# Kernel tuning notes

Measured on AMD Instinct MI355X. Metric: run time of the kernel, lower is better.

The kernel has to match this reference:

```python
import jax, jax.numpy as jnp
import numpy as np

EPS_L2 = 1e-6
EPS_RMS = 1e-6

def _dw_causal(x, w):
    # depthwise causal conv: x [B,L,C], w [C,K] (torch Conv1d weight [C,1,K] squeezed)
    K = w.shape[1]
    L = x.shape[1]
    xp = jnp.pad(x, ((0, 0), (K - 1, 0), (0, 0)))
    out = jnp.zeros_like(x)
    for j in range(K):  # K=4, fixed small kernel
        out = out + w[:, j] * xp[:, j:j + L, :]
    return out

def _qkv_conv(x, dw, pw):
    # depthwise causal conv -> pointwise 1x1 conv -> SiLU
    return jax.nn.silu(_dw_causal(x, dw) @ pw.T)

def _l2n(x):
    return x / (jnp.linalg.norm(x, axis=-1, keepdims=True) + EPS_L2)

def setup_inputs() -> dict:
    key = jax.random.key(0)
    B, L, D, M, P, K = 2, 1024, 2048, 2048, 8, 4
    ks = jax.random.split(key, 16)
    inp = {}
    inp['x'] = jax.random.normal(ks[0], (B, L, D), dtype=jnp.float32)
    inp['Wq'] = jax.random.normal(ks[1], (M, D), dtype=jnp.float32) * 0.02
    inp['Wk'] = jax.random.normal(ks[2], (M, D), dtype=jnp.float32) * 0.02
    inp['Wv'] = jax.random.normal(ks[3], (M, D), dtype=jnp.float32) * 0.02
    inp['q_dw'] = jax.random.normal(ks[4], (M, K), dtype=jnp.float32) * 0.1
    inp['k_dw'] = jax.random.normal(ks[5], (M, K), dtype=jnp.float32) * 0.1
    inp['v_dw'] = jax.random.normal(ks[6], (M, K), dtype=jnp.float32) * 0.1
    inp['q_pw'] = jax.random.normal(ks[7], (M, M), dtype=jnp.float32) * 0.02
    inp['k_pw'] = jax.random.normal(ks[8], (M, M), dtype=jnp.float32) * 0.02
    inp['v_pw'] = jax.random.normal(ks[9], (M, M), dtype=jnp.float32) * 0.02
    inp['pk'] = jax.random.normal(ks[10], (P, M), dtype=jnp.float32) * 0.02
    inp['pv'] = jax.random.normal(ks[11], (P, M), dtype=jnp.float32) * 0.02
    inp['mlp_w1'] = jnp.eye(M, dtype=jnp.float32) * 0.1
    inp['mlp_w2'] = jnp.eye(M, dtype=jnp.float32) * 0.1
    inp['eta_w'] = jnp.zeros((1, D), dtype=jnp.float32)
    inp['eta_b'] = jnp.full((1,), 2.0, dtype=jnp.float32)
    inp['theta_w'] = jnp.zeros((1, D), dtype=jnp.float32)
    inp['theta_b'] = jnp.full((1,), -1.0, dtype=jnp.float32)
    inp['alpha_w'] = jnp.zeros((1, D), dtype=jnp.float32)
    inp['alpha_b'] = jnp.full((1,), -2.0, dtype=jnp.float32)
    inp['gate_w'] = jax.random.normal(ks[12], (M, M), dtype=jnp.float32) * 0.02
    inp['gate_b'] = jnp.zeros((M,), dtype=jnp.float32)
    inp['out_w'] = jax.random.normal(ks[13], (D, M), dtype=jnp.float32) * 0.02
    inp['ln_w'] = jnp.ones((D,), dtype=jnp.float32)
    inp['mem_state'] = jnp.zeros((M, M), dtype=jnp.float32)
    inp['sur_state'] = jnp.zeros((M, M), dtype=jnp.float32)
    return inp

def reference(x, Wq, Wk, Wv, q_dw, q_pw, k_dw, k_pw, v_dw, v_pw, pk, pv,
              mlp_w1, mlp_w2, eta_w, eta_b, theta_w, theta_b, alpha_w, alpha_b,
              gate_w, gate_b, out_w, ln_w, mem_state, sur_state):
    B, L, D = x.shape
    M = Wq.shape[0]
    P = pk.shape[0]
    # projections + causal depthwise-separable convs + SiLU
    q = _qkv_conv(x @ Wq.T, q_dw, q_pw)
    k = _qkv_conv(x @ Wk.T, k_dw, k_pw)
    v = _qkv_conv(x @ Wv.T, v_dw, v_pw)
    q = _l2n(q)
    k = _l2n(k)
    # data-dependent eta/theta/alpha from mean-pooled input, scalarized
    x_pooled = x.mean(axis=1)  # [B, D]
    eta = jax.nn.sigmoid(x_pooled @ eta_w.T + eta_b).mean()
    theta = jax.nn.sigmoid(x_pooled @ theta_w.T + theta_b).mean()
    alpha = jax.nn.sigmoid(x_pooled @ alpha_w.T + alpha_b).mean()
    # persistent memory tokens
    pk_n = _l2n(pk)
    k_wp = jnp.concatenate([jnp.broadcast_to(pk_n[None], (B, P, M)), k], axis=1)
    v_wp = jnp.concatenate([jnp.broadcast_to(pv[None], (B, P, M)), v], axis=1)
    # test-time memory update (torch.no_grad block -> stop_gradient)
    pred = jnp.einsum('blm,mh->blh', k, mem_state)
    err = v - pred
    momentary = jnp.einsum('bld,blh->dh', k, err) / (B * L)
    new_surprise = eta * sur_state + theta * momentary
    new_memory = (1.0 - alpha) * mem_state + new_surprise
    snapshot = jax.lax.stop_gradient(new_memory)
    # retrieval: linear memory + deep memory MLP
    linear_ret = jnp.einsum('blm,mh->blh', q, snapshot)
    mlp_ret = jax.nn.silu(q @ mlp_w1.T) @ mlp_w2.T
    retrieved = linear_ret + mlp_ret
    # causal attention with always-visible persistent tokens
    scores = jnp.einsum('blm,bpm->blp', q, k_wp) / jnp.sqrt(jnp.float32(M))
    col = jnp.arange(P + L)
    row = jnp.arange(L)
    mask = (col[None, :] < P) | ((col[None, :] - P) <= row[:, None])  # [L, P+L]
    scores = jnp.where(mask[None], scores, -jnp.inf)
    attn = jax.nn.softmax(scores.astype(jnp.float32), axis=-1).astype(x.dtype)
    context = jnp.einsum('blp,bpm->blm', attn, v_wp)
    retrieved = retrieved + context
    # gated output projection + residual + RMSNorm
    gate = jax.nn.sigmoid(retrieved @ gate_w.T + gate_b)
    out = x + (gate * retrieved) @ out_w.T
    rms = jnp.sqrt(jnp.mean(out * out, axis=-1, keepdims=True) + EPS_RMS)
    return (out / rms) * ln_w
```

## Files before the change

### kernel.cpp

```cpp
#include <hip/hip_runtime.h>
#include <hip/hip_bf16.h>


#define NROWS 2048
#define MD    2048
#define PL    1032
#define PLP   1152
#define NM    4194304

using bf16x8 = __attribute__((ext_vector_type(8))) __bf16;
using f32x4  = __attribute__((ext_vector_type(4))) float;
using u16x8  = __attribute__((ext_vector_type(8))) unsigned short;

__device__ __forceinline__ unsigned short f2bf(float f) {
    union { float f; unsigned int u; } c; c.f = f;
    unsigned int u = c.u;
    return (unsigned short)((u + 0x7fffu + ((u >> 16) & 1u)) >> 16);
}
__device__ __forceinline__ float bf2f(unsigned short h) {
    union { float f; unsigned int u; } c; c.u = ((unsigned int)h) << 16;
    return c.f;
}
__device__ __forceinline__ float ldf(const float* p) { return *p; }
__device__ __forceinline__ float ldf(const unsigned short* p) { return bf2f(*p); }
__device__ __forceinline__ float sigm(float x) { return 1.f / (1.f + __expf(-x)); }
__device__ __forceinline__ float silu(float x) { return x / (1.f + __expf(-x)); }

__device__ __forceinline__ float block_reduce_sum(float v) {
    __shared__ float ws[4];
    #pragma unroll
    for (int o = 32; o > 0; o >>= 1) v += __shfl_down(v, o);
    __syncthreads();
    if ((threadIdx.x & 63) == 0) ws[threadIdx.x >> 6] = v;
    __syncthreads();
    return (ws[0] + ws[1]) + (ws[2] + ws[3]);
}
__device__ __forceinline__ float block_reduce_max(float v) {
    __shared__ float wm[4];
    #pragma unroll
    for (int o = 32; o > 0; o >>= 1) v = fmaxf(v, __shfl_down(v, o));
    __syncthreads();
    if ((threadIdx.x & 63) == 0) wm[threadIdx.x >> 6] = v;
    __syncthreads();
    return fmaxf(fmaxf(wm[0], wm[1]), fmaxf(wm[2], wm[3]));
}

__device__ __forceinline__ void load_lds16(const unsigned short* g, unsigned short* l) {
    __builtin_amdgcn_global_load_lds(
        (const __attribute__((address_space(1))) unsigned int*)g,
        (__attribute__((address_space(3))) unsigned int*)l, 16, 0, 0);
}
__device__ __forceinline__ void raw_barrier() {
    __asm__ volatile("" ::: "memory");
    __builtin_amdgcn_s_barrier();
    __asm__ volatile("" ::: "memory");
}
__device__ __forceinline__ void epi_store(int epi, float* Cf, unsigned short* Ch,
                                          long off, float v) {
    if (epi == 0)      Cf[off] = v;
    else if (epi == 1) Cf[off] += v;
    else if (epi == 2) Ch[off] = f2bf(v);
    else               Ch[off] = f2bf(silu(v));
}

__global__ __launch_bounds__(256) void gemm_nt(
    const unsigned short* __restrict__ A, const unsigned short* __restrict__ Bm,
    void* __restrict__ Cv, int Mc, int K, long sA, long sB, long sCb, int epiPack)
{
    __shared__ unsigned short As[2][8192];
    __shared__ unsigned short Bs[2][4096];
    const int tid = threadIdx.x, lane = tid & 63, w = tid >> 6;
    const int l16 = lane & 15, quad = lane >> 4;
    const int wr = (w >> 1) * 64, wc = (w & 1) * 32;
    const long rowBase = (long)blockIdx.y * 128;
    const long colBase = (long)blockIdx.x * 64;
    const unsigned short* Ap = A + (long)blockIdx.z * sA;
    const unsigned short* Bp = Bm + (long)blockIdx.z * sB;
    const int epi = (epiPack >> (blockIdx.z * 4)) & 15;
    const int r8 = lane >> 3;
    const int cg = (lane & 7) ^ r8;

    const unsigned short* gA[4]; const unsigned short* gB[2];
    unsigned short* lA[4]; unsigned short* lB[2];
    #pragma unroll
    for (int t = 0; t < 4; ++t) {
        int ch = w * 4 + t;
        gA[t] = Ap + (rowBase + ch * 8 + r8) * (long)K + cg * 8;
        lA[t] = &As[0][ch * 512];
    }
    #pragma unroll
    for (int t = 0; t < 2; ++t) {
        int ch = w * 2 + t;
        gB[t] = Bp + (colBase + ch * 8 + r8) * (long)K + cg * 8;
        lB[t] = &Bs[0][ch * 512];
    }

    f32x4 acc[4][2] = {};
    #pragma unroll
    for (int t = 0; t < 4; ++t) { load_lds16(gA[t], lA[t]); gA[t] += 64; }
    #pragma unroll
    for (int t = 0; t < 2; ++t) { load_lds16(gB[t], lB[t]); gB[t] += 64; }

    const int nIter = K >> 6;
    for (int it = 0; it < nIter; ++it) {
        const int cb = it & 1;
        if (it + 1 < nIter) {
            const int nb = cb ^ 1;
            #pragma unroll
            for (int t = 0; t < 4; ++t) { load_lds16(gA[t], lA[t] + nb * 8192); gA[t] += 64; }
            #pragma unroll
            for (int t = 0; t < 2; ++t) { load_lds16(gB[t], lB[t] + nb * 4096); gB[t] += 64; }
            __builtin_amdgcn_s_waitcnt(0xF76);
        } else {
            __builtin_amdgcn_s_waitcnt(0xF70);
        }
        raw_barrier();
        const unsigned short* Ac = As[cb];
        const unsigned short* Bc = Bs[cb];
        #pragma unroll
        for (int ks = 0; ks < 2; ++ks) {
            const int cl = ((ks * 4 + quad) ^ (l16 & 7)) * 8;
            bf16x8 af[4], bfr[2];
            #pragma unroll
            for (int i = 0; i < 4; ++i)
                af[i] = *(const bf16x8*)&Ac[(wr + i * 16 + l16) * 64 + cl];
            #pragma unroll
            for (int j = 0; j < 2; ++j)
                bfr[j] = *(const bf16x8*)&Bc[(wc + j * 16 + l16) * 64 + cl];
            #pragma unroll
            for (int i = 0; i < 4; ++i)
                #pragma unroll
                for (int j = 0; j < 2; ++j)
                    acc[i][j] = __builtin_amdgcn_mfma_f32_16x16x32_bf16(af[i], bfr[j], acc[i][j], 0, 0, 0);
        }
        raw_barrier();
    }

    char* Cb = (char*)Cv + (long)blockIdx.z * sCb;
    float* Cf = (float*)Cb;
    unsigned short* Ch = (unsigned short*)Cb;
    #pragma unroll
    for (int i = 0; i < 4; ++i)
        #pragma unroll
        for (int r = 0; r < 4; ++r) {
            long gr = rowBase + wr + i * 16 + quad * 4 + r;
            #pragma unroll
            for (int j = 0; j < 2; ++j) {
                long gc = colBase + wc + j * 16 + l16;
                epi_store(epi, Cf, Ch, gr * (long)Mc + gc, acc[i][j][r]);
            }
        }
}

#define G256_RD_A(p)                                                            \
    _Pragma("unroll") for (int fr = 0; fr < 2; ++fr)                            \
    _Pragma("unroll") for (int ks = 0; ks < 2; ++ks)                            \
        af[fr][ks] = *(const bf16x8*)&Ac[(wr + ((p) * 2 + fr) * 16 + l16) * 64  \
                                         + ((ks * 4 + quad) ^ (l16 & 7)) * 8];
#define G256_MFMA(p)                                                            \
    __builtin_amdgcn_s_setprio(1);                                              \
    _Pragma("unroll") for (int ks = 0; ks < 2; ++ks)                            \
    _Pragma("unroll") for (int fr = 0; fr < 2; ++fr)                            \
    _Pragma("unroll") for (int fc = 0; fc < 4; ++fc)                            \
        acc[(p) * 2 + fr][fc] = __builtin_amdgcn_mfma_f32_16x16x32_bf16(        \
            af[fr][ks], bfr[fc][ks], acc[(p) * 2 + fr][fc], 0, 0, 0);           \
    __builtin_amdgcn_s_setprio(0);
#define G256_STG_A(h)                                                           \
    do { load_lds16(gA[h][0], &Anx[lofs[h][0]]); gA[h][0] += 64;                \
         load_lds16(gA[h][1], &Anx[lofs[h][1]]); gA[h][1] += 64; } while (0)
#define G256_STG_B(h)                                                           \
    do { load_lds16(gB[h][0], &Bnx[lofs[h][0]]); gB[h][0] += 64;                \
         load_lds16(gB[h][1], &Bnx[lofs[h][1]]); gB[h][1] += 64; } while (0)

__global__ __launch_bounds__(512, 2) void gemm_nt_256(
    const unsigned short* __restrict__ A, const unsigned short* __restrict__ Bm,
    void* __restrict__ Cv, int Mc, int K, long sA, long sB, long sCb, int epiPack)
{
    __shared__ unsigned short As[2][16384];
    __shared__ unsigned short Bs[2][16384];
    const int tid = threadIdx.x, lane = tid & 63, w = tid >> 6;
    const int l16 = lane & 15, quad = lane >> 4;
    const int wr = (w >> 2) * 128, wc = (w & 3) * 64;
    const long rowBase = (long)blockIdx.y * 256;
    const long colBase = (long)blockIdx.x * 256;
    const unsigned short* Ap = A + (long)blockIdx.z * sA;
    const unsigned short* Bp = Bm + (long)blockIdx.z * sB;
    const int epi = (epiPack >> (blockIdx.z * 4)) & 15;
    const int r8 = lane >> 3;
    const int cg = (lane & 7) ^ r8;

    const unsigned short* gA[2][2]; const unsigned short* gB[2][2];
    int lofs[2][2];
    #pragma unroll
    for (int h = 0; h < 2; ++h)
        #pragma unroll
        for (int j = 0; j < 2; ++j) {
            const int rowOff = h * 128 + j * 64 + w * 8 + r8;
            gA[h][j] = Ap + (rowBase + rowOff) * (long)K + cg * 8;
            gB[h][j] = Bp + (colBase + rowOff) * (long)K + cg * 8;
            lofs[h][j] = (h * 128 + j * 64 + w * 8) * 64;
        }

    const int nT = K >> 6;
    f32x4 acc[8][4] = {};

    #pragma unroll
    for (int h = 0; h < 2; ++h)
        #pragma unroll
        for (int j = 0; j < 2; ++j) { load_lds16(gA[h][j], &As[0][lofs[h][j]]); gA[h][j] += 64; }
    #pragma unroll
    for (int h = 0; h < 2; ++h)
        #pragma unroll
        for (int j = 0; j < 2; ++j) { load_lds16(gB[h][j], &Bs[0][lofs[h][j]]); gB[h][j] += 64; }
    if (nT > 1) {
        #pragma unroll
        for (int h = 0; h < 2; ++h)
            #pragma unroll
            for (int j = 0; j < 2; ++j) { load_lds16(gB[h][j], &Bs[1][lofs[h][j]]); gB[h][j] += 64; }
        __builtin_amdgcn_s_waitcnt(0x0F74);
    } else {
        __builtin_amdgcn_s_waitcnt(0x0F70);
    }
    raw_barrier();

    for (int t = 0; t < nT; ++t) {
        const int cb = t & 1;
        const unsigned short* Ac = As[cb];
        const unsigned short* Bc = Bs[cb];
        unsigned short* Anx = As[cb ^ 1];
        unsigned short* Bnx = Bs[cb];
        const bool stA = (t + 1 < nT);
        const bool stB = (t + 2 < nT);
        bf16x8 bfr[4][2];
        bf16x8 af[2][2];

        #pragma unroll
        for (int fc = 0; fc < 4; ++fc)
            #pragma unroll
            for (int ks = 0; ks < 2; ++ks)
                bfr[fc][ks] = *(const bf16x8*)&Bc[(wc + fc * 16 + l16) * 64
                                                 + ((ks * 4 + quad) ^ (l16 & 7)) * 8];
        G256_RD_A(0)
        if (stA) G256_STG_A(0);
        raw_barrier();
        G256_MFMA(0)
        raw_barrier();

        G256_RD_A(1)
        if (stA) G256_STG_A(1);
        raw_barrier();
        G256_MFMA(1)
        raw_barrier();

        G256_RD_A(2)
        if (stB) G256_STG_B(0);
        raw_barrier();
        G256_MFMA(2)
        raw_barrier();

        G256_RD_A(3)
        if (stB) {
            G256_STG_B(1);
            __builtin_amdgcn_s_waitcnt(0x0F74);
        } else {
            __builtin_amdgcn_s_waitcnt(0x0F70);
        }
        raw_barrier();
        G256_MFMA(3)
        raw_barrier();
    }

    char* Cb = (char*)Cv + (long)blockIdx.z * sCb;
    float* Cf = (float*)Cb;
    unsigned short* Ch = (unsigned short*)Cb;
    #pragma unroll
    for (int i = 0; i < 8; ++i)
        #pragma unroll
        for (int r = 0; r < 4; ++r) {
            long gr = rowBase + wr + i * 16 + quad * 4 + r;
            #pragma unroll
            for (int j = 0; j < 4; ++j) {
                long gc = colBase + wc + j * 16 + l16;
                epi_store(epi, Cf, Ch, gr * (long)Mc + gc, acc[i][j][r]);
            }
        }
}

template <typename TS>
__global__ void k_transpose(const TS* __restrict__ src, unsigned short* __restrict__ dst,
                            int R, int C, int dstLd, int dstOff, long sSrc, long sDst)
{
    __shared__ float tile[32][33];
    const TS* sp = src + (long)blockIdx.z * sSrc;
    unsigned short* dp = dst + (long)blockIdx.z * sDst;
    int c0 = blockIdx.x * 32, r0 = blockIdx.y * 32;
    int tx = threadIdx.x, ty = threadIdx.y;
    #pragma unroll
    for (int i = 0; i < 4; ++i)
        tile[ty + i * 8][tx] = ldf(&sp[(long)(r0 + ty + i * 8) * C + c0 + tx]);
    __syncthreads();
    #pragma unroll
    for (int i = 0; i < 4; ++i)
        dp[(long)(c0 + ty + i * 8) * dstLd + dstOff + r0 + tx] = f2bf(tile[tx][ty + i * 8]);
}

__global__ void k_errT_kT(const unsigned short* __restrict__ vf, const float* __restrict__ pred,
                          const unsigned short* __restrict__ k_bf, unsigned short* __restrict__ eT)
{
    __shared__ float tile[32][33];
    int z = blockIdx.z;
    int c0 = blockIdx.x * 32, r0 = blockIdx.y * 32;
    int tx = threadIdx.x, ty = threadIdx.y;
    #pragma unroll
    for (int i = 0; i < 4; ++i) {
        long idx = (long)(r0 + ty + i * 8) * MD + c0 + tx;
        tile[ty + i * 8][tx] = (z == 0) ? (bf2f(vf[idx]) - pred[idx]) : bf2f(k_bf[idx]);
    }
    __syncthreads();
    unsigned short* dst = eT + (long)z * NM;
    #pragma unroll
    for (int i = 0; i < 4; ++i)
        dst[(long)(c0 + ty + i * 8) * MD + r0 + tx] = f2bf(tile[tx][ty + i * 8]);
}

__global__ void k_snapT(const float* __restrict__ mem, const float* __restrict__ sur,
                        const float* __restrict__ momT, const float* __restrict__ scal,
                        unsigned short* __restrict__ dst)
{
    __shared__ float tile[32][33];
    float eta = scal[0], theta = scal[1], alpha = scal[2];
    int h0 = blockIdx.y * 32, d0 = blockIdx.x * 32;
    int tx = threadIdx.x, ty = threadIdx.y;
    #pragma unroll
    for (int i = 0; i < 4; ++i) {
        long idx = (long)(d0 + ty + i * 8) * MD + h0 + tx;
        tile[ty + i * 8][tx] = (1.f - alpha) * mem[idx] + eta * sur[idx];
    }
    __syncthreads();
    #pragma unroll
    for (int i = 0; i < 4; ++i) {
        long oidx = (long)(h0 + ty + i * 8) * MD + d0 + tx;
        dst[oidx] = f2bf(tile[tx][ty + i * 8] + theta * (1.f / 2048.f) * momT[oidx]);
    }
}

__global__ void k_cvt_multi(const float* s0, const float* s1, const float* s2, const float* s3,
                            const float* s4, const float* s5, const float* s6, const float* s7,
                            unsigned short* d0, unsigned short* d1, unsigned short* d2, unsigned short* d3,
                            unsigned short* d4, unsigned short* d5, unsigned short* d6, unsigned short* d7)
{
    int seg = blockIdx.x >> 11;
    const float* s; unsigned short* d;
    switch (seg) {
        case 0: s = s0; d = d0; break;  case 1: s = s1; d = d1; break;
        case 2: s = s2; d = d2; break;  case 3: s = s3; d = d3; break;
        case 4: s = s4; d = d4; break;  case 5: s = s5; d = d5; break;
        case 6: s = s6; d = d6; break;  default: s = s7; d = d7; break;
    }
    long idx = ((long)(blockIdx.x & 2047) * 256 + threadIdx.x) * 8;
    float4 a = *(const float4*)(s + idx);
    float4 b = *(const float4*)(s + idx + 4);
    u16x8 o;
    o[0] = f2bf(a.x); o[1] = f2bf(a.y); o[2] = f2bf(a.z); o[3] = f2bf(a.w);
    o[4] = f2bf(b.x); o[5] = f2bf(b.y); o[6] = f2bf(b.z); o[7] = f2bf(b.w);
    *(u16x8*)(d + idx) = o;
}

__global__ void k_dwconv(const unsigned short* __restrict__ tproj,
                         const float* __restrict__ qdw, const float* __restrict__ kdw,
                         const float* __restrict__ vdw, unsigned short* __restrict__ conv)
{
    long u = (long)blockIdx.x * 256 + threadIdx.x;
    long flat = u * 8;
    int z = (int)(flat >> 22);
    int rem = (int)(flat & (NM - 1));
    int n = rem >> 11, m = rem & 2047;
    int l = n & 1023;
    const float* dw = (z == 0) ? qdw : (z == 1) ? kdw : vdw;
    const unsigned short* src = tproj + (long)n * 6144 + z * 2048 + m;
    float4 dwv[8];
    #pragma unroll
    for (int e = 0; e < 8; ++e) dwv[e] = *(const float4*)(dw + (m + e) * 4);
    float acc[8] = {};
    #pragma unroll
    for (int j = 0; j < 4; ++j) {
        int dl = j - 3;
        if (l + dl >= 0) {
            u16x8 r = *(const u16x8*)(src + (long)dl * 6144);
            #pragma unroll
            for (int e = 0; e < 8; ++e)
                acc[e] += ((const float*)&dwv[e])[j] * bf2f(r[e]);
        }
    }
    u16x8 o;
    #pragma unroll
    for (int e = 0; e < 8; ++e) o[e] = f2bf(acc[e]);
    *(u16x8*)(conv + (long)z * NM + (long)n * 2048 + m) = o;
}

__global__ void k_post_qkv(const float* __restrict__ t_big, unsigned short* __restrict__ q_bf,
                           unsigned short* __restrict__ k_bf, unsigned short* __restrict__ vf,
                           unsigned short* __restrict__ kwp)
{
    int bid = blockIdx.x, z = bid >> 11, n = bid & 2047;
    const float* row = t_big + (long)z * NM + (long)n * 2048;
    int t = threadIdx.x;
    float4 a = *(const float4*)(row + t * 8);
    float4 b = *(const float4*)(row + t * 8 + 4);
    float v[8] = {silu(a.x), silu(a.y), silu(a.z), silu(a.w),
                  silu(b.x), silu(b.y), silu(b.z), silu(b.w)};
    if (z == 2) {
        u16x8 o;
        #pragma unroll
        for (int e = 0; e < 8; ++e) o[e] = f2bf(v[e]);
        *(u16x8*)(vf + (long)n * 2048 + t * 8) = o;
        return;
    }
    float ss = 0.f;
    #pragma unroll
    for (int e = 0; e < 8; ++e) ss += v[e] * v[e];
    ss = block_reduce_sum(ss);
    float inv = 1.f / (sqrtf(ss) + 1e-6f);
    u16x8 o;
    #pragma unroll
    for (int e = 0; e < 8; ++e) o[e] = f2bf(v[e] * inv);
    if (z == 0) {
        *(u16x8*)(q_bf + (long)n * 2048 + t * 8) = o;
    } else {
        *(u16x8*)(k_bf + (long)n * 2048 + t * 8) = o;
        int bb = n >> 10, l = n & 1023;
        *(u16x8*)(kwp + ((long)bb * PLP + 8 + l) * MD + t * 8) = o;
    }
}

__global__ void k_misc(const float* __restrict__ pk, const float* __restrict__ pv,
                       unsigned short* __restrict__ kwp, unsigned short* __restrict__ vwpT)
{
    int bid = blockIdx.x, t = threadIdx.x;
    if (bid < 8) {
        const float* row = pk + bid * MD;
        float4 a = *(const float4*)(row + t * 8);
        float4 b = *(const float4*)(row + t * 8 + 4);
        float v[8] = {a.x, a.y, a.z, a.w, b.x, b.y, b.z, b.w};
        float ss = 0.f;
        #pragma unroll
        for (int e = 0; e < 8; ++e) ss += v[e] * v[e];
        ss = block_reduce_sum(ss);
        float inv = 1.f / (sqrtf(ss) + 1e-6f);
        u16x8 o;
        #pragma unroll
        for (int e = 0; e < 8; ++e) o[e] = f2bf(v[e] * inv);
        *(u16x8*)(kwp + (long)bid * MD + t * 8) = o;
        *(u16x8*)(kwp + (long)PLP * MD + (long)bid * MD + t * 8) = o;
    } else if (bid < 72) {
        int i = (bid - 8) * 256 + t;
        int m = i >> 3, pp = i & 7;
        unsigned short h = f2bf(pv[pp * MD + m]);
        vwpT[(long)m * PLP + pp] = h;
        vwpT[(long)MD * PLP + (long)m * PLP + pp] = h;
    } else if (bid < 312) {
        long flat = ((long)(bid - 72) * 256 + t) * 8;
        int b = (int)(flat / 245760);
        int r = (int)(flat % 245760);
        int j = 1032 + (r >> 11), m = r & 2047;
        u16x8 zz = {};
        *(u16x8*)(kwp + ((long)b * PLP + j) * MD + m) = zz;
    } else {
        long flat = ((long)(bid - 312) * 256 + t) * 8;
        int bm = (int)(flat / 120);
        int o = (int)(flat % 120);
        u16x8 zz = {};
        *(u16x8*)(vwpT + (long)bm * PLP + 1032 + o) = zz;
    }
}

__global__ void k_pooled(const float* __restrict__ x, const float* __restrict__ ew,
                         const float* __restrict__ tw, const float* __restrict__ aw,
                         float* __restrict__ dots) {
    int b = blockIdx.y;
    long base = (long)b * 1024 * MD;
    long start = (long)blockIdx.x * 8192;
    float s0 = 0, s1 = 0, s2 = 0;
    for (int s = 0; s < 32; ++s) {
        long f = start + threadIdx.x + (long)s * 256;
        float xv = x[base + f];
        int d = (int)(f & (MD - 1));
        s0 += xv * ew[d]; s1 += xv * tw[d]; s2 += xv * aw[d];
    }
    s0 = block_reduce_sum(s0);
    if (threadIdx.x == 0) atomicAdd(&dots[0 + b], s0);
    s1 = block_reduce_sum(s1);
    if (threadIdx.x == 0) atomicAdd(&dots[2 + b], s1);
    s2 = block_reduce_sum(s2);
    if (threadIdx.x == 0) atomicAdd(&dots[4 + b], s2);
}
__global__ void k_scal_fin(const float* __restrict__ dots, const float* __restrict__ eb,
                           const float* __restrict__ tb, const float* __restrict__ ab,
                           float* __restrict__ scal) {
    if (threadIdx.x == 0 && blockIdx.x == 0) {
        const float invL = 1.f / 1024.f;
        float e = 0, th = 0, al = 0;
        for (int b = 0; b < 2; ++b) {
            e  += sigm(dots[0 + b] * invL + eb[0]);
            th += sigm(dots[2 + b] * invL + tb[0]);
            al += sigm(dots[4 + b] * invL + ab[0]);
        }
        scal[0] = e * 0.5f; scal[1] = th * 0.5f; scal[2] = al * 0.5f;
    }
}

__global__ void k_addcvt(const float* __restrict__ a, const float* __restrict__ b,
                         unsigned short* __restrict__ o) {
    long i = ((long)blockIdx.x * 256 + threadIdx.x) * 8;
    float4 a0 = *(const float4*)(a + i), a1 = *(const float4*)(a + i + 4);
    float4 b0 = *(const float4*)(b + i), b1 = *(const float4*)(b + i + 4);
    u16x8 r;
    r[0] = f2bf(a0.x + b0.x); r[1] = f2bf(a0.y + b0.y); r[2] = f2bf(a0.z + b0.z); r[3] = f2bf(a0.w + b0.w);
    r[4] = f2bf(a1.x + b1.x); r[5] = f2bf(a1.y + b1.y); r[6] = f2bf(a1.z + b1.z); r[7] = f2bf(a1.w + b1.w);
    *(u16x8*)(o + i) = r;
}
__global__ void k_gate8(const float* __restrict__ pre, const float* __restrict__ gb,
                        const float* __restrict__ ret, const float* __restrict__ mlp2,
                        unsigned short* __restrict__ o) {
    long i = ((long)blockIdx.x * 256 + threadIdx.x) * 8;
    int m = (int)(i & (MD - 1));
    float4 p0 = *(const float4*)(pre + i),  p1 = *(const float4*)(pre + i + 4);
    float4 r0 = *(const float4*)(ret + i),  r1 = *(const float4*)(ret + i + 4);
    float4 q0 = *(const float4*)(mlp2 + i), q1 = *(const float4*)(mlp2 + i + 4);
    float4 g0 = *(const float4*)(gb + m),   g1 = *(const float4*)(gb + m + 4);
    u16x8 r;
    r[0] = f2bf(sigm(p0.x + g0.x) * (r0.x + q0.x));
    r[1] = f2bf(sigm(p0.y + g0.y) * (r0.y + q0.y));
    r[2] = f2bf(sigm(p0.z + g0.z) * (r0.z + q0.z));
    r[3] = f2bf(sigm(p0.w + g0.w) * (r0.w + q0.w));
    r[4] = f2bf(sigm(p1.x + g1.x) * (r1.x + q1.x));
    r[5] = f2bf(sigm(p1.y + g1.y) * (r1.y + q1.y));
    r[6] = f2bf(sigm(p1.z + g1.z) * (r1.z + q1.z));
    r[7] = f2bf(sigm(p1.w + g1.w) * (r1.w + q1.w));
    *(u16x8*)(o + i) = r;
}

__global__ void k_softmax(const float* __restrict__ S, unsigned short* __restrict__ attn) {
    int l = blockIdx.x, b = blockIdx.y;
    long base = ((long)b * 1024 + l) * PLP;
    int nvis = 8 + l + 1;
    const float scale = 0.022097086912079608f;
    int t = threadIdx.x;
    float vals[5];
    float mx = -1e30f;
    #pragma unroll
    for (int s = 0; s < 5; ++s) {
        int j = t + s * 256;
        float v = -1e30f;
        if (j < nvis) v = S[base + j] * scale;
        vals[s] = v;
        mx = fmaxf(mx, v);
    }
    mx = block_reduce_max(mx);
    float sum = 0.f;
    #pragma unroll
    for (int s = 0; s < 5; ++s) {
        int j = t + s * 256;
        float e = 0.f;
        if (j < nvis) e = __expf(vals[s] - mx);
        vals[s] = e; sum += e;
    }
    sum = block_reduce_sum(sum);
    float inv = 1.f / sum;
    #pragma unroll
    for (int s = 0; s < 5; ++s) {
        int j = t + s * 256;
        if (j < PLP) attn[base + j] = f2bf(vals[s] * inv);
    }
}

__global__ void k_final(const float* __restrict__ x, const float* __restrict__ y,
                        const float* __restrict__ lnw, float* __restrict__ out) {
    int n = blockIdx.x;
    long base = (long)n * MD;
    int t = threadIdx.x;
    float4 a0 = *(const float4*)(x + base + t * 8), a1 = *(const float4*)(x + base + t * 8 + 4);
    float4 b0 = *(const float4*)(y + base + t * 8), b1 = *(const float4*)(y + base + t * 8 + 4);
    float v[8] = {a0.x + b0.x, a0.y + b0.y, a0.z + b0.z, a0.w + b0.w,
                  a1.x + b1.x, a1.y + b1.y, a1.z + b1.z, a1.w + b1.w};
    float ss = 0.f;
    #pragma unroll
    for (int e = 0; e < 8; ++e) ss += v[e] * v[e];
    ss = block_reduce_sum(ss);
    float inv = rsqrtf(ss * (1.f / 2048.f) + 1e-6f);
    float4 w0 = *(const float4*)(lnw + t * 8), w1 = *(const float4*)(lnw + t * 8 + 4);
    float4 o0 = {v[0] * inv * w0.x, v[1] * inv * w0.y, v[2] * inv * w0.z, v[3] * inv * w0.w};
    float4 o1 = {v[4] * inv * w1.x, v[5] * inv * w1.y, v[6] * inv * w1.z, v[7] * inv * w1.w};
    *(float4*)(out + base + t * 8) = o0;
    *(float4*)(out + base + t * 8 + 4) = o1;
}

static inline void gemm64(hipStream_t st, const void* A, const void* B, void* C,
                          int Mc, int K, long sA, long sB, long sCb,
                          int gx, int gy, int gz, int epiPack) {
    hipLaunchKernelGGL(gemm_nt, dim3(gx, gy, gz), dim3(256), 0, st,
                       (const unsigned short*)A, (const unsigned short*)B, C,
                       Mc, K, sA, sB, sCb, epiPack);
}
static inline void gemm256(hipStream_t st, const void* A, const void* B, void* C,
                           int Mc, int K, long sA, long sB, long sCb,
                           int gx, int gy, int gz, int epiPack) {
    hipLaunchKernelGGL(gemm_nt_256, dim3(gx, gy, gz), dim3(512), 0, st,
                       (const unsigned short*)A, (const unsigned short*)B, C,
                       Mc, K, sA, sB, sCb, epiPack);
}

extern "C" void kernel_launch(void* const* d_in, const int* in_sizes, int n_in,
                              void* d_out, int out_size, void* d_ws, size_t ws_size,
                              hipStream_t stream) {
    const float* x    = (const float*)d_in[0];
    const float* Wq   = (const float*)d_in[1];
    const float* Wk   = (const float*)d_in[2];
    const float* Wv   = (const float*)d_in[3];
    const float* qdw  = (const float*)d_in[4];
    const float* kdw  = (const float*)d_in[5];
    const float* vdw  = (const float*)d_in[6];
    const float* qpw  = (const float*)d_in[7];
    const float* kpw  = (const float*)d_in[8];
    const float* vpw  = (const float*)d_in[9];
    const float* pk   = (const float*)d_in[10];
    const float* pv   = (const float*)d_in[11];
    const float* mw1  = (const float*)d_in[12];
    const float* mw2  = (const float*)d_in[13];
    const float* etaw = (const float*)d_in[14];
    const float* etab = (const float*)d_in[15];
    const float* thw  = (const float*)d_in[16];
    const float* thb  = (const float*)d_in[17];
    const float* alw  = (const float*)d_in[18];
    const float* alb  = (const float*)d_in[19];
    const float* gw   = (const float*)d_in[20];
    const float* gb   = (const float*)d_in[21];
    const float* ow   = (const float*)d_in[22];
    const float* lnw  = (const float*)d_in[23];
    const float* mem  = (const float*)d_in[24];
    const float* sur  = (const float*)d_in[25];
    float* out = (float*)d_out;

    char* ws = (char*)d_ws;
    const size_t MB = 1024 * 1024;
    float* dots = (float*)ws;
    float* scal = (float*)(ws + 1024);
    float*          t0f  = (float*)(ws + 4096);
    float*          t1f  = t0f + NM;
    float*          t2f  = t0f + 2 * NM;
    unsigned short* tproj = (unsigned short*)t0f;
    float*          retf = (float*)(ws + 4096 + 48 * MB);
    unsigned short* k_bf = (unsigned short*)(ws + 4096 + 64 * MB);
    unsigned short* q_bf = k_bf + NM;
    unsigned short* qc   = k_bf + 2 * NM;
    unsigned short* g_bf = k_bf;
    unsigned short* x_bf = (unsigned short*)(ws + 4096 + 88 * MB);
    unsigned short* vf   = x_bf;
    unsigned short* attn = x_bf;
    unsigned short* wQKV = (unsigned short*)(ws + 4096 + 96 * MB);
    unsigned short* conv = wQKV;
    unsigned short* kwp  = wQKV;
    unsigned short* vwpT = kwp + (long)2 * PLP * MD;
    unsigned short* wPW  = (unsigned short*)(ws + 4096 + 120 * MB);
    unsigned short* eT   = wPW;
    unsigned short* kT   = eT + NM;
    unsigned short* gw_bf = wPW;
    unsigned short* ow_bf = wPW + NM;
    unsigned short* wMem  = (unsigned short*)(ws + 4096 + 144 * MB);
    unsigned short* wMlp1 = wMem + NM;
    unsigned short* wSnap = wMem;
    unsigned short* wMlp2 = wMem + NM;

    const dim3 b256(256);
    const dim3 bT(32, 8);

    hipMemsetAsync(dots, 0, 256, stream);
    hipLaunchKernelGGL(k_pooled, dim3(256, 2), b256, 0, stream, x, etaw, thw, alw, dots);
    hipLaunchKernelGGL(k_scal_fin, dim3(1), dim3(64), 0, stream, dots, etab, thb, alb, scal);
    hipLaunchKernelGGL(k_cvt_multi, dim3(16384), b256, 0, stream,
                       x, Wq, Wk, Wv, qpw, kpw, vpw, mw1,
                       x_bf, wQKV, wQKV + NM, wQKV + 2 * (long)NM,
                       wPW, wPW + NM, wPW + 2 * (long)NM, wMlp1);
    hipLaunchKernelGGL(k_transpose<float>, dim3(64, 64, 1), bT, 0, stream,
                       mem, wMem, MD, MD, MD, 0, 0L, 0L);
    gemm256(stream, x_bf, wQKV, tproj, 6144, MD, 0, 0, 0, 24, 8, 1, 2);
    hipLaunchKernelGGL(k_dwconv, dim3(6144), b256, 0, stream, tproj, qdw, kdw, vdw, conv);
    gemm256(stream, conv, wPW, t0f, MD, MD, NM, NM, (long)NM * 4, 8, 8, 3, 0);
    hipLaunchKernelGGL(k_misc, dim3(552), b256, 0, stream, pk, pv, kwp, vwpT);
    hipLaunchKernelGGL(k_post_qkv, dim3(6144), b256, 0, stream, t0f, q_bf, k_bf, vf, kwp);
    hipLaunchKernelGGL(k_transpose<unsigned short>, dim3(64, 32, 2), bT, 0, stream,
                       vf, vwpT, 1024, MD, PLP, 8, (long)1024 * MD, (long)MD * PLP);
    gemm256(stream, k_bf, wMem, t0f, MD, MD, NM, NM,
            (long)((char*)qc - (char*)t0f), 8, 8, 2, 0x30);
    hipLaunchKernelGGL(k_errT_kT, dim3(64, 64, 2), bT, 0, stream, vf, t0f, k_bf, eT);
    gemm64(stream, eT, kT, t2f, MD, MD, 0, 0, 0, 32, 16, 1, 0);
    hipLaunchKernelGGL(k_snapT, dim3(64, 64), bT, 0, stream, mem, sur, t2f, scal, wSnap);
    hipLaunchKernelGGL(k_cvt_multi, dim3(6144), b256, 0, stream,
                       mw2, gw, ow, mw2, mw2, mw2, mw2, mw2,
                       wMlp2, gw_bf, ow_bf, wMlp2, wMlp2, wMlp2, wMlp2, wMlp2);
    gemm256(stream, q_bf, wSnap, retf, MD, MD, NM, NM,
            (long)((char*)t1f - (char*)retf), 8, 8, 2, 0);
    gemm64(stream, q_bf, kwp, t2f, PLP, MD,
           (long)1024 * MD, (long)PLP * MD, (long)1024 * PLP * 4, 18, 8, 2, 0);
    hipLaunchKernelGGL(k_softmax, dim3(1024, 2), b256, 0, stream, t2f, attn);
    gemm64(stream, attn, vwpT, retf, MD, PLP,
           (long)1024 * PLP, (long)MD * PLP, (long)1024 * MD * 4, 32, 8, 2, 0x11);
    hipLaunchKernelGGL(k_addcvt, dim3(2048), b256, 0, stream, retf, t1f, qc);
    gemm64(stream, qc, gw_bf, t0f, MD, MD, 0, 0, 0, 32, 16, 1, 0);
    hipLaunchKernelGGL(k_gate8, dim3(2048), b256, 0, stream, t0f, gb, retf, t1f, g_bf);
    gemm64(stream, g_bf, ow_bf, t0f, MD, MD, 0, 0, 0, 32, 16, 1, 0);
    hipLaunchKernelGGL(k_final, dim3(2048), b256, 0, stream, x, t0f, lnw, out);
}
```

Measured before the change: 816.1 us.

## Fuse SiLU, residual-add and gating into GEMM epilogues; add 128x128 GEMM tile

The pointwise-conv GEMM now applies SiLU and writes bf16 directly instead of fp32, so k_post_qkv reads half the bytes and the V path needs no separate conversion. The context GEMM epilogue accumulates into retf and also emits the bf16 sum with the MLP output, which replaces k_addcvt. The gate GEMM epilogue applies sigmoid and bias and multiplies by the retrieved value, which replaces k_gate8. A new 128x128-tile GEMM kernel is used for the two memory GEMMs, which raises data reuse per block but lowers the block count. Each fused epilogue does scattered scalar reads of extra fp32 arrays, and q and k now pass through bf16 before L2 normalisation, which changes rounding slightly.

```diff
diff --git a/kernel.cpp b/kernel.cpp
--- a/kernel.cpp
+++ b/kernel.cpp
@@ -56,16 +56,22 @@
     __asm__ volatile("" ::: "memory");
 }
 __device__ __forceinline__ void epi_store(int epi, float* Cf, unsigned short* Ch,
-                                          long off, float v) {
+                                          long off, int gc, float v,
+                                          const float* gbp, const float* r1z,
+                                          const float* r2z, unsigned short* qhz) {
     if (epi == 0)      Cf[off] = v;
     else if (epi == 1) Cf[off] += v;
     else if (epi == 2) Ch[off] = f2bf(v);
-    else               Ch[off] = f2bf(silu(v));
+    else if (epi == 3) Ch[off] = f2bf(silu(v));
+    else if (epi == 4) Ch[off] = f2bf(sigm(v + gbp[gc]) * (r1z[off] + r2z[off]));
+    else { float r = Cf[off] + v; Cf[off] = r; qhz[off] = f2bf(r + r2z[off]); }
 }
 
 __global__ __launch_bounds__(256) void gemm_nt(
     const unsigned short* __restrict__ A, const unsigned short* __restrict__ Bm,
-    void* __restrict__ Cv, int Mc, int K, long sA, long sB, long sCb, int epiPack)
+    void* __restrict__ Cv, int Mc, int K, long sA, long sB, long sCb, int epiPack,
+    const float* __restrict__ gbp, const float* __restrict__ r1,
+    const float* __restrict__ r2, unsigned short* __restrict__ qh)
 {
     __shared__ unsigned short As[2][8192];
     __shared__ unsigned short Bs[2][4096];
@@ -139,6 +145,10 @@
     char* Cb = (char*)Cv + (long)blockIdx.z * sCb;
     float* Cf = (float*)Cb;
     unsigned short* Ch = (unsigned short*)Cb;
+    const long zel = (long)blockIdx.z * (sCb >> 2);
+    const float* r1z = r1 + zel;
+    const float* r2z = r2 + zel;
+    unsigned short* qhz = qh + zel;
     #pragma unroll
     for (int i = 0; i < 4; ++i)
         #pragma unroll
@@ -147,7 +157,94 @@
             #pragma unroll
             for (int j = 0; j < 2; ++j) {
                 long gc = colBase + wc + j * 16 + l16;
-                epi_store(epi, Cf, Ch, gr * (long)Mc + gc, acc[i][j][r]);
+                epi_store(epi, Cf, Ch, gr * (long)Mc + gc, (int)gc, acc[i][j][r],
+                          gbp, r1z, r2z, qhz);
+            }
+        }
+}
+
+__global__ __launch_bounds__(256) void gemm_nt_big(
+    const unsigned short* __restrict__ A, const unsigned short* __restrict__ Bm,
+    void* __restrict__ Cv, int Mc, int K, long sA, long sB, long sCb, int epiPack)
+{
+    __shared__ unsigned short As[2][8192];
+    __shared__ unsigned short Bs[2][8192];
+    const int tid = threadIdx.x, lane = tid & 63, w = tid >> 6;
+    const int l16 = lane & 15, quad = lane >> 4;
+    const int wr = (w >> 1) * 64, wc = (w & 1) * 64;
+    const long rowBase = (long)blockIdx.y * 128;
+    const long colBase = (long)blockIdx.x * 128;
+    const unsigned short* Ap = A + (long)blockIdx.z * sA;
+    const unsigned short* Bp = Bm + (long)blockIdx.z * sB;
+    const int epi = (epiPack >> (blockIdx.z * 4)) & 15;
+    const int r8 = lane >> 3;
+    const int cg = (lane & 7) ^ r8;
+
+    const unsigned short* gA[4]; const unsigned short* gB[4];
+    unsigned short* lA[4]; unsigned short* lB[4];
+    #pragma unroll
+    for (int t = 0; t < 4; ++t) {
+        int ch = w * 4 + t;
+        gA[t] = Ap + (rowBase + ch * 8 + r8) * (long)K + cg * 8;
+        lA[t] = &As[0][ch * 512];
+        gB[t] = Bp + (colBase + ch * 8 + r8) * (long)K + cg * 8;
+        lB[t] = &Bs[0][ch * 512];
+    }
+
+    f32x4 acc[4][4] = {};
+    #pragma unroll
+    for (int t = 0; t < 4; ++t) { load_lds16(gA[t], lA[t]); gA[t] += 64; }
+    #pragma unroll
+    for (int t = 0; t < 4; ++t) { load_lds16(gB[t], lB[t]); gB[t] += 64; }
+
+    const int nIter = K >> 6;
+    for (int it = 0; it < nIter; ++it) {
+        const int cb = it & 1;
+        if (it + 1 < nIter) {
+            const int nb = cb ^ 1;
+            #pragma unroll
+            for (int t = 0; t < 4; ++t) { load_lds16(gA[t], lA[t] + nb * 8192); gA[t] += 64; }
+            #pragma unroll
+            for (int t = 0; t < 4; ++t) { load_lds16(gB[t], lB[t] + nb * 8192); gB[t] += 64; }
+            __builtin_amdgcn_s_waitcnt(0xF78);
+        } else {
+            __builtin_amdgcn_s_waitcnt(0xF70);
+        }
+        raw_barrier();
+        const unsigned short* Ac = As[cb];
+        const unsigned short* Bc = Bs[cb];
+        #pragma unroll
+        for (int ks = 0; ks < 2; ++ks) {
+            const int cl = ((ks * 4 + quad) ^ (l16 & 7)) * 8;
+            bf16x8 af[4], bfr[4];
+            #pragma unroll
+            for (int i = 0; i < 4; ++i)
+                af[i] = *(const bf16x8*)&Ac[(wr + i * 16 + l16) * 64 + cl];
+            #pragma unroll
+            for (int j = 0; j < 4; ++j)
+                bfr[j] = *(const bf16x8*)&Bc[(wc + j * 16 + l16) * 64 + cl];
+            #pragma unroll
+            for (int i = 0; i < 4; ++i)
+                #pragma unroll
+                for (int j = 0; j < 4; ++j)
+                    acc[i][j] = __builtin_amdgcn_mfma_f32_16x16x32_bf16(af[i], bfr[j], acc[i][j], 0, 0, 0);
+        }
+        raw_barrier();
+    }
+
+    char* Cb = (char*)Cv + (long)blockIdx.z * sCb;
+    float* Cf = (float*)Cb;
+    unsigned short* Ch = (unsigned short*)Cb;
+    #pragma unroll
+    for (int i = 0; i < 4; ++i)
+        #pragma unroll
+        for (int r = 0; r < 4; ++r) {
+            long gr = rowBase + wr + i * 16 + quad * 4 + r;
+            #pragma unroll
+            for (int j = 0; j < 4; ++j) {
+                long gc = colBase + wc + j * 16 + l16;
+                epi_store(epi, Cf, Ch, gr * (long)Mc + gc, (int)gc, acc[i][j][r],
+                          nullptr, nullptr, nullptr, nullptr);
             }
         }
 }
@@ -281,7 +378,8 @@
             #pragma unroll
             for (int j = 0; j < 4; ++j) {
                 long gc = colBase + wc + j * 16 + l16;
-                epi_store(epi, Cf, Ch, gr * (long)Mc + gc, acc[i][j][r]);
+                epi_store(epi, Cf, Ch, gr * (long)Mc + gc, (int)gc, acc[i][j][r],
+                          nullptr, nullptr, nullptr, nullptr);
             }
         }
 }
@@ -398,24 +496,16 @@
     *(u16x8*)(conv + (long)z * NM + (long)n * 2048 + m) = o;
 }
 
-__global__ void k_post_qkv(const float* __restrict__ t_big, unsigned short* __restrict__ q_bf,
-                           unsigned short* __restrict__ k_bf, unsigned short* __restrict__ vf,
-                           unsigned short* __restrict__ kwp)
+__global__ void k_post_qkv(const unsigned short* __restrict__ tbf, unsigned short* __restrict__ q_bf,
+                           unsigned short* __restrict__ k_bf, unsigned short* __restrict__ kwp)
 {
     int bid = blockIdx.x, z = bid >> 11, n = bid & 2047;
-    const float* row = t_big + (long)z * NM + (long)n * 2048;
+    const unsigned short* row = tbf + (long)z * NM + (long)n * 2048;
     int t = threadIdx.x;
-    float4 a = *(const float4*)(row + t * 8);
-    float4 b = *(const float4*)(row + t * 8 + 4);
-    float v[8] = {silu(a.x), silu(a.y), silu(a.z), silu(a.w),
-                  silu(b.x), silu(b.y), silu(b.z), silu(b.w)};
-    if (z == 2) {
-        u16x8 o;
-        #pragma unroll
-        for (int e = 0; e < 8; ++e) o[e] = f2bf(v[e]);
-        *(u16x8*)(vf + (long)n * 2048 + t * 8) = o;
-        return;
-    }
+    u16x8 iv = *(const u16x8*)(row + t * 8);
+    float v[8];
+    #pragma unroll
+    for (int e = 0; e < 8; ++e) v[e] = bf2f(iv[e]);
     float ss = 0.f;
     #pragma unroll
     for (int e = 0; e < 8; ++e) ss += v[e] * v[e];
@@ -509,37 +599,6 @@
     }
 }
 
-__global__ void k_addcvt(const float* __restrict__ a, const float* __restrict__ b,
-                         unsigned short* __restrict__ o) {
-    long i = ((long)blockIdx.x * 256 + threadIdx.x) * 8;
-    float4 a0 = *(const float4*)(a + i), a1 = *(const float4*)(a + i + 4);
-    float4 b0 = *(const float4*)(b + i), b1 = *(const float4*)(b + i + 4);
-    u16x8 r;
-    r[0] = f2bf(a0.x + b0.x); r[1] = f2bf(a0.y + b0.y); r[2] = f2bf(a0.z + b0.z); r[3] = f2bf(a0.w + b0.w);
-    r[4] = f2bf(a1.x + b1.x); r[5] = f2bf(a1.y + b1.y); r[6] = f2bf(a1.z + b1.z); r[7] = f2bf(a1.w + b1.w);
-    *(u16x8*)(o + i) = r;
-}
-__global__ void k_gate8(const float* __restrict__ pre, const float* __restrict__ gb,
-                        const float* __restrict__ ret, const float* __restrict__ mlp2,
-                        unsigned short* __restrict__ o) {
-    long i = ((long)blockIdx.x * 256 + threadIdx.x) * 8;
-    int m = (int)(i & (MD - 1));
-    float4 p0 = *(const float4*)(pre + i),  p1 = *(const float4*)(pre + i + 4);
-    float4 r0 = *(const float4*)(ret + i),  r1 = *(const float4*)(ret + i + 4);
-    float4 q0 = *(const float4*)(mlp2 + i), q1 = *(const float4*)(mlp2 + i + 4);
-    float4 g0 = *(const float4*)(gb + m),   g1 = *(const float4*)(gb + m + 4);
-    u16x8 r;
-    r[0] = f2bf(sigm(p0.x + g0.x) * (r0.x + q0.x));
-    r[1] = f2bf(sigm(p0.y + g0.y) * (r0.y + q0.y));
-    r[2] = f2bf(sigm(p0.z + g0.z) * (r0.z + q0.z));
-    r[3] = f2bf(sigm(p0.w + g0.w) * (r0.w + q0.w));
-    r[4] = f2bf(sigm(p1.x + g1.x) * (r1.x + q1.x));
-    r[5] = f2bf(sigm(p1.y + g1.y) * (r1.y + q1.y));
-    r[6] = f2bf(sigm(p1.z + g1.z) * (r1.z + q1.z));
-    r[7] = f2bf(sigm(p1.w + g1.w) * (r1.w + q1.w));
-    *(u16x8*)(o + i) = r;
-}
-
 __global__ void k_softmax(const float* __restrict__ S, unsigned short* __restrict__ attn) {
     int l = blockIdx.x, b = blockIdx.y;
     long base = ((long)b * 1024 + l) * PLP;
@@ -597,8 +656,17 @@
 
 static inline void gemm64(hipStream_t st, const void* A, const void* B, void* C,
                           int Mc, int K, long sA, long sB, long sCb,
-                          int gx, int gy, int gz, int epiPack) {
+                          int gx, int gy, int gz, int epiPack,
+                          const float* gbp = nullptr, const float* r1 = nullptr,
+                          const float* r2 = nullptr, unsigned short* qh = nullptr) {
     hipLaunchKernelGGL(gemm_nt, dim3(gx, gy, gz), dim3(256), 0, st,
+                       (const unsigned short*)A, (const unsigned short*)B, C,
+                       Mc, K, sA, sB, sCb, epiPack, gbp, r1, r2, qh);
+}
+static inline void gemm128(hipStream_t st, const void* A, const void* B, void* C,
+                           int Mc, int K, long sA, long sB, long sCb,
+                           int gx, int gy, int gz, int epiPack) {
+    hipLaunchKernelGGL(gemm_nt_big, dim3(gx, gy, gz), dim3(256), 0, st,
                        (const unsigned short*)A, (const unsigned short*)B, C,
                        Mc, K, sA, sB, sCb, epiPack);
 }
@@ -649,13 +717,14 @@
     float*          t1f  = t0f + NM;
     float*          t2f  = t0f + 2 * NM;
     unsigned short* tproj = (unsigned short*)t0f;
+    unsigned short* t_bf  = (unsigned short*)t0f;
+    unsigned short* vf    = t_bf + 2 * (long)NM;
     float*          retf = (float*)(ws + 4096 + 48 * MB);
     unsigned short* k_bf = (unsigned short*)(ws + 4096 + 64 * MB);
     unsigned short* q_bf = k_bf + NM;
     unsigned short* qc   = k_bf + 2 * NM;
     unsigned short* g_bf = k_bf;
     unsigned short* x_bf = (unsigned short*)(ws + 4096 + 88 * MB);
-    unsigned short* vf   = x_bf;
     unsigned short* attn = x_bf;
     unsigned short* wQKV = (unsigned short*)(ws + 4096 + 96 * MB);
     unsigned short* conv = wQKV;
@@ -685,29 +754,29 @@
                        mem, wMem, MD, MD, MD, 0, 0L, 0L);
     gemm256(stream, x_bf, wQKV, tproj, 6144, MD, 0, 0, 0, 24, 8, 1, 2);
     hipLaunchKernelGGL(k_dwconv, dim3(6144), b256, 0, stream, tproj, qdw, kdw, vdw, conv);
-    gemm256(stream, conv, wPW, t0f, MD, MD, NM, NM, (long)NM * 4, 8, 8, 3, 0);
+    gemm256(stream, conv, wPW, t_bf, MD, MD, NM, NM, (long)NM * 2, 8, 8, 3, 0x333);
     hipLaunchKernelGGL(k_misc, dim3(552), b256, 0, stream, pk, pv, kwp, vwpT);
-    hipLaunchKernelGGL(k_post_qkv, dim3(6144), b256, 0, stream, t0f, q_bf, k_bf, vf, kwp);
+    hipLaunchKernelGGL(k_post_qkv, dim3(4096), b256, 0, stream, t_bf, q_bf, k_bf, kwp);
     hipLaunchKernelGGL(k_transpose<unsigned short>, dim3(64, 32, 2), bT, 0, stream,
                        vf, vwpT, 1024, MD, PLP, 8, (long)1024 * MD, (long)MD * PLP);
-    gemm256(stream, k_bf, wMem, t0f, MD, MD, NM, NM,
-            (long)((char*)qc - (char*)t0f), 8, 8, 2, 0x30);
+    gemm128(stream, k_bf, wMem, t0f, MD, MD, NM, NM,
+            (long)((char*)qc - (char*)t0f), 16, 16, 2, 0x30);
     hipLaunchKernelGGL(k_errT_kT, dim3(64, 64, 2), bT, 0, stream, vf, t0f, k_bf, eT);
     gemm64(stream, eT, kT, t2f, MD, MD, 0, 0, 0, 32, 16, 1, 0);
     hipLaunchKernelGGL(k_snapT, dim3(64, 64), bT, 0, stream, mem, sur, t2f, scal, wSnap);
     hipLaunchKernelGGL(k_cvt_multi, dim3(6144), b256, 0, stream,
                        mw2, gw, ow, mw2, mw2, mw2, mw2, mw2,
                        wMlp2, gw_bf, ow_bf, wMlp2, wMlp2, wMlp2, wMlp2, wMlp2);
-    gemm256(stream, q_bf, wSnap, retf, MD, MD, NM, NM,
-            (long)((char*)t1f - (char*)retf), 8, 8, 2, 0);
+    gemm128(stream, q_bf, wSnap, retf, MD, MD, NM, NM,
+            (long)((char*)t1f - (char*)retf), 16, 16, 2, 0);
     gemm64(stream, q_bf, kwp, t2f, PLP, MD,
            (long)1024 * MD, (long)PLP * MD, (long)1024 * PLP * 4, 18, 8, 2, 0);
     hipLaunchKernelGGL(k_softmax, dim3(1024, 2), b256, 0, stream, t2f, attn);
     gemm64(stream, attn, vwpT, retf, MD, PLP,
-           (long)1024 * PLP, (long)MD * PLP, (long)1024 * MD * 4, 32, 8, 2, 0x11);
-    hipLaunchKernelGGL(k_addcvt, dim3(2048), b256, 0, stream, retf, t1f, qc);
-    gemm64(stream, qc, gw_bf, t0f, MD, MD, 0, 0, 0, 32, 16, 1, 0);
-    hipLaunchKernelGGL(k_gate8, dim3(2048), b256, 0, stream, t0f, gb, retf, t1f, g_bf);
+           (long)1024 * PLP, (long)MD * PLP, (long)1024 * MD * 4, 32, 8, 2, 0x55,
+           nullptr, retf, t1f, qc);
+    gemm64(stream, qc, gw_bf, g_bf, MD, MD, 0, 0, 0, 32, 16, 1, 4,
+           gb, retf, t1f, nullptr);
     gemm64(stream, g_bf, ow_bf, t0f, MD, MD, 0, 0, 0, 32, 16, 1, 0);
     hipLaunchKernelGGL(k_final, dim3(2048), b256, 0, stream, x, t0f, lnw, out);
 }
```

New measurement: 773.7 us. 1.05x faster.
